# Kernel optimization log

Measured on AMD Instinct MI355X. Metric: run time of the kernel, lower is better.

The kernel has to match this reference:

```python
import jax, jax.numpy as jnp
import numpy as np

DIM = 512
HEADS = 8
SCALE = (DIM // HEADS) ** -0.5  # 0.125
B, H, W = 1, 64, 64  # square spatial grid required by torch matmul broadcasting


def setup_inputs() -> dict:
    key = jax.random.key(0)
    ks = jax.random.split(key, 7)
    s = DIM ** -0.5
    return {
        "x": jax.random.normal(ks[0], (B, H, W, DIM), dtype=jnp.float32),
        "mask": 0,  # sentinel for None (mask must be None in the original)
        "Wq": jax.random.normal(ks[1], (DIM, DIM), dtype=jnp.float32) * s,
        "bq": jax.random.normal(ks[2], (DIM,), dtype=jnp.float32) * 0.01,
        "Wk": jax.random.normal(ks[3], (DIM, DIM), dtype=jnp.float32) * s,
        "bk": jax.random.normal(ks[4], (DIM,), dtype=jnp.float32) * 0.01,
        "Wv": jax.random.normal(ks[5], (DIM, DIM), dtype=jnp.float32) * s,
        "bv": jax.random.normal(ks[6], (DIM,), dtype=jnp.float32) * 0.01,
    }


def reference(x, mask, Wq, bq, Wk, bk, Wv, bv):
    # Linear projections (nn.Linear: x @ W.T + b)
    q = jnp.einsum('bhwc,oc->bhwo', x, Wq) + bq
    k = jnp.einsum('bhwc,oc->bhwo', x, Wk) + bk
    v = jnp.einsum('bhwc,oc->bhwo', x, Wv) + bv
    # Faithful to torch.einsum('bhwc,bpqd->bhwpq', q, k): c and d are each
    # summed independently => outer product of channel-sums. [b,h,w,p,q]
    weights = jnp.einsum('bhwc,bpqd->bhwpq', q, k)
    # dropout is identity in eval mode; then scale and softmax over last axis
    weights = jax.nn.softmax(weights * SCALE, axis=-1)
    # torch matmul broadcasting: [b,h,w,p,q] @ [b,p,q,d] -> [b,h,w,p,d]
    attn = jnp.matmul(weights, v)
    return attn
```

## Files before the change

### kernel.cpp

```cpp
#include <hip/hip_runtime.h>

typedef _Float16 half8 __attribute__((ext_vector_type(8)));
typedef float f32x4 __attribute__((ext_vector_type(4)));
typedef float float4_t __attribute__((ext_vector_type(4)));
typedef unsigned int uint32x2 __attribute__((ext_vector_type(2)));

#define DIM 512
#define S 64
#define NROW 4096
#define LDSW 88

__device__ __forceinline__ void bar_lds() {
    asm volatile("s_waitcnt lgkmcnt(0)" ::: "memory");
    __builtin_amdgcn_s_barrier();
    asm volatile("" ::: "memory");
}

__global__ void colsum_vt_kernel(const float* __restrict__ Wq, const float* __restrict__ bq,
                                 const float* __restrict__ Wk, const float* __restrict__ bk,
                                 float* __restrict__ part,
                                 float* __restrict__ pbias,
                                 const float* __restrict__ X,
                                 const float* __restrict__ Wv,
                                 const float* __restrict__ bv,
                                 _Float16* __restrict__ Vs) {
    int bid = blockIdx.x;
    if (bid < 8) {
        int sel = bid >> 2, qr = bid & 3;
        const float* W = sel ? Wk : Wq;
        const float* bias = sel ? bk : bq;
        int t = threadIdx.x;
        int c0 = t, c1 = t + 256;
        float s0 = 0.f, s1 = 0.f;
        const float* Wr = W + (size_t)qr * 128 * DIM;
        for (int o = 0; o < 128; ++o) {
            s0 += Wr[o * DIM + c0];
            s1 += Wr[o * DIM + c1];
        }
        part[(sel * 4 + qr) * 512 + c0] = s0;
        part[(sel * 4 + qr) * 512 + c1] = s1;
        if (qr == 0) {
            float bs = bias[c0] + bias[c1];
#pragma unroll
            for (int off = 32; off >= 1; off >>= 1) bs += __shfl_xor(bs, off);
            __shared__ float red[4];
            if ((t & 63) == 0) red[t >> 6] = bs;
            __syncthreads();
            if (t == 0) pbias[sel] = red[0] + red[1] + red[2] + red[3];
        }
        return;
    }
    int b2 = bid - 8;
    int mb = b2 & 255;
    int cb = b2 >> 8;
    int wv_ = threadIdx.x >> 6;
    int lane = threadIdx.x & 63;
    int lr = lane & 15;
    int lg = lane >> 4;
    int row0 = mb * 16;
    int col0 = cb * 256 + wv_ * 64;

    f32x4 acc[4];
#pragma unroll
    for (int n = 0; n < 4; n++) acc[n] = (f32x4){0.f, 0.f, 0.f, 0.f};

    for (int kk = 0; kk < 16; ++kk) {
        int kbase = kk * 32 + lg * 8;
        const float4_t* pa = (const float4_t*)(X + (size_t)(row0 + lr) * DIM + kbase);
        float4_t x0 = pa[0], x1 = pa[1];
        half8 a;
#pragma unroll
        for (int i = 0; i < 4; i++) { a[i] = (_Float16)x0[i]; a[i + 4] = (_Float16)x1[i]; }
#pragma unroll
        for (int n = 0; n < 4; n++) {
            const float4_t* pb = (const float4_t*)(Wv + (size_t)(col0 + n * 16 + lr) * DIM + kbase);
            float4_t b0 = pb[0], b1 = pb[1];
            half8 hb;
#pragma unroll
            for (int i = 0; i < 4; i++) { hb[i] = (_Float16)b0[i]; hb[i + 4] = (_Float16)b1[i]; }
            acc[n] = __builtin_amdgcn_mfma_f32_16x16x32_f16(a, hb, acc[n], 0, 0, 0);
        }
    }
    int w   = mb >> 2;
    int s_  = (mb & 3) >> 1;
    int lg2 = ((mb & 3) * 2 + (lg >> 1)) & 3;
    int e0  = (lg & 1) * 4;
#pragma unroll
    for (int n = 0; n < 4; n++) {
        int d = col0 + n * 16 + lr;
        int dt = d >> 4;
        float bvc = bv[d];
        _Float16 tmp[4];
#pragma unroll
        for (int r = 0; r < 4; r++) tmp[r] = (_Float16)(acc[n][r] + bvc);
        int idx8 = (((w * 32 + dt) * 2 + s_) * 4 + lg2) * 16 + lr;
        __builtin_nontemporal_store(*(uint32x2*)tmp, (uint32x2*)(Vs + (size_t)idx8 * 8 + e0));
    }
}

__global__ void rowdot_kernel(const float* __restrict__ X,
                              const float* __restrict__ part,
                              const float* __restrict__ pbias,
                              float* __restrict__ a_arr,
                              float* __restrict__ ks_arr) {
    int wave = threadIdx.x >> 6;
    int lane = threadIdx.x & 63;
    int row = blockIdx.x * 4 + wave;
    const float4_t* xr = (const float4_t*)(X + (size_t)row * DIM) + lane * 2;
    float4_t x0 = xr[0], x1 = xr[1];
    float sq = 0.f, sk = 0.f;
#pragma unroll
    for (int qr = 0; qr < 4; ++qr) {
        const float4_t* pq = (const float4_t*)(part + qr * 512) + lane * 2;
        const float4_t* pk = (const float4_t*)(part + 2048 + qr * 512) + lane * 2;
        float4_t q0 = pq[0], q1 = pq[1];
        float4_t k0 = pk[0], k1 = pk[1];
#pragma unroll
        for (int i = 0; i < 4; i++) {
            sq += x0[i] * q0[i] + x1[i] * q1[i];
            sk += x0[i] * k0[i] + x1[i] * k1[i];
        }
    }
#pragma unroll
    for (int off = 32; off >= 1; off >>= 1) {
        sq += __shfl_xor(sq, off);
        sk += __shfl_xor(sk, off);
    }
    if (lane == 0) {
        a_arr[row]  = (sq + pbias[0]) * 0.125f;
        ks_arr[row] = sk + pbias[1];
    }
}

__global__ __launch_bounds__(256) void attn_main_kernel(
        const float* __restrict__ a_arr,
        const float* __restrict__ ks_arr,
        const _Float16* __restrict__ Vs,
        float* __restrict__ out) {
    __shared__ __align__(16) char smem[32768];
    _Float16* Wsm = (_Float16*)smem;
    char* Osm = smem;

    int b = blockIdx.x;
    int l = (b & 7) * 256 + (b >> 3);
    int w = l >> 5;
    int h0 = (l & 31) * 2;
    int t = threadIdx.x;
    int wv_ = t >> 6, lane = t & 63;
    int lr = lane & 15, lg = lane >> 4;

    const half8* Vg = (const half8*)Vs;

    half8 vfr[4][2][2];
#pragma unroll
    for (int j2 = 0; j2 < 4; ++j2)
#pragma unroll
        for (int c = 0; c < 2; ++c) {
            int dt = j2 * 8 + wv_ * 2 + c;
            int g0 = ((w * 32 + dt) * 2) * 64 + lane;
            vfr[j2][c][0] = Vg[g0];
            vfr[j2][c][1] = Vg[g0 + 64];
        }

    float a0 = a_arr[h0 * 64 + w];
    float a1 = a_arr[(h0 + 1) * 64 + w];

    for (int hh = 0; hh < 2; ++hh) {
        float a = hh ? a1 : a0;
        int hw = (h0 + hh) * 64 + w;

        bar_lds();

        {
            int p = t >> 2, c = t & 3;
            const float4_t* kp = (const float4_t*)(ks_arr + p * 64 + c * 16);
            float4_t k0 = kp[0], k1 = kp[1], k2 = kp[2], k3 = kp[3];
            float L[16];
#pragma unroll
            for (int i = 0; i < 4; i++) {
                L[i] = a * k0[i]; L[4 + i] = a * k1[i];
                L[8 + i] = a * k2[i]; L[12 + i] = a * k3[i];
            }
            float m = L[0];
#pragma unroll
            for (int i = 1; i < 16; i++) m = fmaxf(m, L[i]);
            m = fmaxf(m, __shfl_xor(m, 1));
            m = fmaxf(m, __shfl_xor(m, 2));
            float e[16];
            float sum = 0.f;
#pragma unroll
            for (int i = 0; i < 16; i++) { e[i] = __expf(L[i] - m); sum += e[i]; }
            sum += __shfl_xor(sum, 1);
            sum += __shfl_xor(sum, 2);
            float r = 1.0f / sum;
            half8 hv0, hv1;
#pragma unroll
            for (int i = 0; i < 8; i++) {
                hv0[i] = (_Float16)(e[i] * r);
                hv1[i] = (_Float16)(e[8 + i] * r);
            }
            *(half8*)&Wsm[p * LDSW + c * 16]     = hv0;
            *(half8*)&Wsm[p * LDSW + c * 16 + 8] = hv1;
        }
        bar_lds();

        half8 wfr[4][2];
#pragma unroll
        for (int pt = 0; pt < 4; ++pt)
#pragma unroll
            for (int s_ = 0; s_ < 2; ++s_)
                wfr[pt][s_] = *(const half8*)&Wsm[(pt * 16 + lr) * LDSW + s_ * 32 + lg * 8];

        char* outb = (char*)(out + (size_t)hw * (64 * DIM));

#pragma unroll
        for (int j2 = 0; j2 < 4; ++j2) {
            f32x4 acc[2][4];
#pragma unroll
            for (int c = 0; c < 2; ++c)
#pragma unroll
                for (int pt = 0; pt < 4; ++pt) acc[c][pt] = (f32x4){0.f, 0.f, 0.f, 0.f};
#pragma unroll
            for (int pt = 0; pt < 4; ++pt) {
                acc[0][pt] = __builtin_amdgcn_mfma_f32_16x16x32_f16(vfr[j2][0][0], wfr[pt][0], acc[0][pt], 0, 0, 0);
                acc[0][pt] = __builtin_amdgcn_mfma_f32_16x16x32_f16(vfr[j2][0][1], wfr[pt][1], acc[0][pt], 0, 0, 0);
                acc[1][pt] = __builtin_amdgcn_mfma_f32_16x16x32_f16(vfr[j2][1][0], wfr[pt][0], acc[1][pt], 0, 0, 0);
                acc[1][pt] = __builtin_amdgcn_mfma_f32_16x16x32_f16(vfr[j2][1][1], wfr[pt][1], acc[1][pt], 0, 0, 0);
            }
            bar_lds();
#pragma unroll
            for (int c = 0; c < 2; ++c)
#pragma unroll
                for (int pt = 0; pt < 4; ++pt) {
                    int p = pt * 16 + lr;
                    int addr = p * 512 + (wv_ * 32 + c * 16 + lg * 4) * 4;
                    addr ^= (p & 7) << 4;
                    *(f32x4*)(Osm + addr) = acc[c][pt];
                }
            bar_lds();
#pragma unroll
            for (int i = 0; i < 8; ++i) {
                int f = i * 4096 + t * 16;
                int row = f >> 9;
                int rb = f ^ ((row & 7) << 4);
                f32x4 val = *(const f32x4*)(Osm + rb);
                __builtin_nontemporal_store(val, (f32x4*)(outb + (size_t)row * 2048 + j2 * 512 + (f & 511)));
            }
        }
    }
}

extern "C" void kernel_launch(void* const* d_in, const int* in_sizes, int n_in,
                              void* d_out, int out_size, void* d_ws, size_t ws_size,
                              hipStream_t stream) {
    const float* x  = (const float*)d_in[0];
    const float* Wq = (const float*)d_in[2];
    const float* bq = (const float*)d_in[3];
    const float* Wk = (const float*)d_in[4];
    const float* bk = (const float*)d_in[5];
    const float* Wv = (const float*)d_in[6];
    const float* bv = (const float*)d_in[7];
    float* out = (float*)d_out;
    char* ws = (char*)d_ws;

    _Float16* Vs  = (_Float16*)ws;
    float* a_arr  = (float*)(ws + 4194304);
    float* ks_arr = (float*)(ws + 4210688);
    float* part   = (float*)(ws + 4227072);
    float* pbias  = (float*)(ws + 4243456);

    colsum_vt_kernel<<<520, 256, 0, stream>>>(Wq, bq, Wk, bk, part, pbias, x, Wv, bv, Vs);
    rowdot_kernel<<<1024, 256, 0, stream>>>(x, part, pbias, a_arr, ks_arr);
    attn_main_kernel<<<2048, 256, 0, stream>>>(a_arr, ks_arr, Vs, out);
}
```

Before: 139.9 us.

## Process one spatial position per block and stream V fragments per tile

The attention kernel now handles one (h,w) position per block instead of two and doubles the grid. V fragments are loaded one d-tile group at a time, just before use, instead of all being preloaded into registers. The launch bound asks for four blocks per CU. The aim is to cut register pressure and raise occupancy so more output stores are in flight, at the cost of re-reading V for every position and recomputing nothing else.

```diff
diff --git a/kernel.cpp b/kernel.cpp
--- a/kernel.cpp
+++ b/kernel.cpp
@@ -132,7 +132,7 @@
     }
 }
 
-__global__ __launch_bounds__(256) void attn_main_kernel(
+__global__ __launch_bounds__(256, 4) void attn_main_kernel(
         const float* __restrict__ a_arr,
         const float* __restrict__ ks_arr,
         const _Float16* __restrict__ Vs,
@@ -142,110 +142,105 @@
     char* Osm = smem;
 
     int b = blockIdx.x;
-    int l = (b & 7) * 256 + (b >> 3);
-    int w = l >> 5;
-    int h0 = (l & 31) * 2;
+    int swz = (b & 7) * 512 + (b >> 3);
+    int w = swz >> 6;
+    int h = swz & 63;
+    int hw = h * 64 + w;
     int t = threadIdx.x;
     int wv_ = t >> 6, lane = t & 63;
     int lr = lane & 15, lg = lane >> 4;
 
     const half8* Vg = (const half8*)Vs;
 
-    half8 vfr[4][2][2];
-#pragma unroll
-    for (int j2 = 0; j2 < 4; ++j2)
-#pragma unroll
-        for (int c = 0; c < 2; ++c) {
-            int dt = j2 * 8 + wv_ * 2 + c;
-            int g0 = ((w * 32 + dt) * 2) * 64 + lane;
-            vfr[j2][c][0] = Vg[g0];
-            vfr[j2][c][1] = Vg[g0 + 64];
-        }
-
-    float a0 = a_arr[h0 * 64 + w];
-    float a1 = a_arr[(h0 + 1) * 64 + w];
-
-    for (int hh = 0; hh < 2; ++hh) {
-        float a = hh ? a1 : a0;
-        int hw = (h0 + hh) * 64 + w;
-
+    int dtb = wv_ * 2;
+    half8 vc0 = Vg[((w * 32 + dtb) * 2 + 0) * 64 + lane];
+    half8 vc1 = Vg[((w * 32 + dtb) * 2 + 1) * 64 + lane];
+    half8 vc2 = Vg[((w * 32 + dtb + 1) * 2 + 0) * 64 + lane];
+    half8 vc3 = Vg[((w * 32 + dtb + 1) * 2 + 1) * 64 + lane];
+
+    float a = a_arr[hw];
+
+    {
+        int p = t >> 2, c = t & 3;
+        const float4_t* kp = (const float4_t*)(ks_arr + p * 64 + c * 16);
+        float4_t k0 = kp[0], k1 = kp[1], k2 = kp[2], k3 = kp[3];
+        float L[16];
+#pragma unroll
+        for (int i = 0; i < 4; i++) {
+            L[i] = a * k0[i]; L[4 + i] = a * k1[i];
+            L[8 + i] = a * k2[i]; L[12 + i] = a * k3[i];
+        }
+        float m = L[0];
+#pragma unroll
+        for (int i = 1; i < 16; i++) m = fmaxf(m, L[i]);
+        m = fmaxf(m, __shfl_xor(m, 1));
+        m = fmaxf(m, __shfl_xor(m, 2));
+        float e[16];
+        float sum = 0.f;
+#pragma unroll
+        for (int i = 0; i < 16; i++) { e[i] = __expf(L[i] - m); sum += e[i]; }
+        sum += __shfl_xor(sum, 1);
+        sum += __shfl_xor(sum, 2);
+        float r = 1.0f / sum;
+        half8 h0, h1;
+#pragma unroll
+        for (int i = 0; i < 8; i++) {
+            h0[i] = (_Float16)(e[i] * r);
+            h1[i] = (_Float16)(e[8 + i] * r);
+        }
+        *(half8*)&Wsm[p * LDSW + c * 16]     = h0;
+        *(half8*)&Wsm[p * LDSW + c * 16 + 8] = h1;
+    }
+    bar_lds();
+
+    half8 wfr[4][2];
+#pragma unroll
+    for (int pt = 0; pt < 4; ++pt)
+#pragma unroll
+        for (int s_ = 0; s_ < 2; ++s_)
+            wfr[pt][s_] = *(const half8*)&Wsm[(pt * 16 + lr) * LDSW + s_ * 32 + lg * 8];
+
+    char* outb = (char*)(out + (size_t)hw * (64 * DIM));
+
+#pragma unroll
+    for (int j2 = 0; j2 < 4; ++j2) {
+        f32x4 acc[2][4];
+#pragma unroll
+        for (int c = 0; c < 2; ++c)
+#pragma unroll
+            for (int pt = 0; pt < 4; ++pt) acc[c][pt] = (f32x4){0.f, 0.f, 0.f, 0.f};
+#pragma unroll
+        for (int pt = 0; pt < 4; ++pt) {
+            acc[0][pt] = __builtin_amdgcn_mfma_f32_16x16x32_f16(vc0, wfr[pt][0], acc[0][pt], 0, 0, 0);
+            acc[0][pt] = __builtin_amdgcn_mfma_f32_16x16x32_f16(vc1, wfr[pt][1], acc[0][pt], 0, 0, 0);
+            acc[1][pt] = __builtin_amdgcn_mfma_f32_16x16x32_f16(vc2, wfr[pt][0], acc[1][pt], 0, 0, 0);
+            acc[1][pt] = __builtin_amdgcn_mfma_f32_16x16x32_f16(vc3, wfr[pt][1], acc[1][pt], 0, 0, 0);
+        }
+        if (j2 < 3) {
+            int dt0 = (j2 + 1) * 8 + dtb;
+            vc0 = Vg[((w * 32 + dt0) * 2 + 0) * 64 + lane];
+            vc1 = Vg[((w * 32 + dt0) * 2 + 1) * 64 + lane];
+            vc2 = Vg[((w * 32 + dt0 + 1) * 2 + 0) * 64 + lane];
+            vc3 = Vg[((w * 32 + dt0 + 1) * 2 + 1) * 64 + lane];
+        }
         bar_lds();
-
-        {
-            int p = t >> 2, c = t & 3;
-            const float4_t* kp = (const float4_t*)(ks_arr + p * 64 + c * 16);
-            float4_t k0 = kp[0], k1 = kp[1], k2 = kp[2], k3 = kp[3];
-            float L[16];
-#pragma unroll
-            for (int i = 0; i < 4; i++) {
-                L[i] = a * k0[i]; L[4 + i] = a * k1[i];
-                L[8 + i] = a * k2[i]; L[12 + i] = a * k3[i];
+#pragma unroll
+        for (int c = 0; c < 2; ++c)
+#pragma unroll
+            for (int pt = 0; pt < 4; ++pt) {
+                int p = pt * 16 + lr;
+                int addr = p * 512 + (wv_ * 32 + c * 16 + lg * 4) * 4;
+                addr ^= (p & 7) << 4;
+                *(f32x4*)(Osm + addr) = acc[c][pt];
             }
-            float m = L[0];
-#pragma unroll
-            for (int i = 1; i < 16; i++) m = fmaxf(m, L[i]);
-            m = fmaxf(m, __shfl_xor(m, 1));
-            m = fmaxf(m, __shfl_xor(m, 2));
-            float e[16];
-            float sum = 0.f;
-#pragma unroll
-            for (int i = 0; i < 16; i++) { e[i] = __expf(L[i] - m); sum += e[i]; }
-            sum += __shfl_xor(sum, 1);
-            sum += __shfl_xor(sum, 2);
-            float r = 1.0f / sum;
-            half8 hv0, hv1;
-#pragma unroll
-            for (int i = 0; i < 8; i++) {
-                hv0[i] = (_Float16)(e[i] * r);
-                hv1[i] = (_Float16)(e[8 + i] * r);
-            }
-            *(half8*)&Wsm[p * LDSW + c * 16]     = hv0;
-            *(half8*)&Wsm[p * LDSW + c * 16 + 8] = hv1;
-        }
         bar_lds();
-
-        half8 wfr[4][2];
-#pragma unroll
-        for (int pt = 0; pt < 4; ++pt)
-#pragma unroll
-            for (int s_ = 0; s_ < 2; ++s_)
-                wfr[pt][s_] = *(const half8*)&Wsm[(pt * 16 + lr) * LDSW + s_ * 32 + lg * 8];
-
-        char* outb = (char*)(out + (size_t)hw * (64 * DIM));
-
-#pragma unroll
-        for (int j2 = 0; j2 < 4; ++j2) {
-            f32x4 acc[2][4];
-#pragma unroll
-            for (int c = 0; c < 2; ++c)
-#pragma unroll
-                for (int pt = 0; pt < 4; ++pt) acc[c][pt] = (f32x4){0.f, 0.f, 0.f, 0.f};
-#pragma unroll
-            for (int pt = 0; pt < 4; ++pt) {
-                acc[0][pt] = __builtin_amdgcn_mfma_f32_16x16x32_f16(vfr[j2][0][0], wfr[pt][0], acc[0][pt], 0, 0, 0);
-                acc[0][pt] = __builtin_amdgcn_mfma_f32_16x16x32_f16(vfr[j2][0][1], wfr[pt][1], acc[0][pt], 0, 0, 0);
-                acc[1][pt] = __builtin_amdgcn_mfma_f32_16x16x32_f16(vfr[j2][1][0], wfr[pt][0], acc[1][pt], 0, 0, 0);
-                acc[1][pt] = __builtin_amdgcn_mfma_f32_16x16x32_f16(vfr[j2][1][1], wfr[pt][1], acc[1][pt], 0, 0, 0);
-            }
-            bar_lds();
-#pragma unroll
-            for (int c = 0; c < 2; ++c)
-#pragma unroll
-                for (int pt = 0; pt < 4; ++pt) {
-                    int p = pt * 16 + lr;
-                    int addr = p * 512 + (wv_ * 32 + c * 16 + lg * 4) * 4;
-                    addr ^= (p & 7) << 4;
-                    *(f32x4*)(Osm + addr) = acc[c][pt];
-                }
-            bar_lds();
-#pragma unroll
-            for (int i = 0; i < 8; ++i) {
-                int f = i * 4096 + t * 16;
-                int row = f >> 9;
-                int rb = f ^ ((row & 7) << 4);
-                f32x4 val = *(const f32x4*)(Osm + rb);
-                __builtin_nontemporal_store(val, (f32x4*)(outb + (size_t)row * 2048 + j2 * 512 + (f & 511)));
-            }
+#pragma unroll
+        for (int i = 0; i < 8; ++i) {
+            int f = i * 4096 + t * 16;
+            int row = f >> 9;
+            int rb = f ^ ((row & 7) << 4);
+            f32x4 val = *(const f32x4*)(Osm + rb);
+            __builtin_nontemporal_store(val, (f32x4*)(outb + (size_t)row * 2048 + j2 * 512 + (f & 511)));
         }
     }
 }
@@ -271,5 +266,5 @@
 
     colsum_vt_kernel<<<520, 256, 0, stream>>>(Wq, bq, Wk, bk, part, pbias, x, Wv, bv, Vs);
     rowdot_kernel<<<1024, 256, 0, stream>>>(x, part, pbias, a_arr, ks_arr);
-    attn_main_kernel<<<2048, 256, 0, stream>>>(a_arr, ks_arr, Vs, out);
-}
+    attn_main_kernel<<<4096, 256, 0, stream>>>(a_arr, ks_arr, Vs, out);
+}
```

New measurement: 144.4 us. 1.03x slower.

## Give each wave a private LDS slice and drop block-wide barriers

Applied to the files above, without the earlier changes.

Repartitions the attention kernel so each wavefront owns 16 rows of p and its own 8KB LDS slice. Each wave computes the softmax weights for its rows, stages them, and transposes output tiles through its private slice, so the s_barrier calls are replaced by lgkmcnt waits plus scheduling barriers. V fragments are now loaded per j2 chunk and prefetched for the next chunk during the second h iteration, which trades register footprint for a reload per chunk. The aim is to remove block-wide synchronisation stalls between the MFMA and store phases. Correctness relies on each wave reading only the LDS data it wrote itself.

```diff
diff --git a/kernel.cpp b/kernel.cpp
--- a/kernel.cpp
+++ b/kernel.cpp
@@ -10,10 +10,10 @@
 #define NROW 4096
 #define LDSW 88
 
-__device__ __forceinline__ void bar_lds() {
+__device__ __forceinline__ void fence_lds() {
+    __builtin_amdgcn_sched_barrier(0);
     asm volatile("s_waitcnt lgkmcnt(0)" ::: "memory");
-    __builtin_amdgcn_s_barrier();
-    asm volatile("" ::: "memory");
+    __builtin_amdgcn_sched_barrier(0);
 }
 
 __global__ void colsum_vt_kernel(const float* __restrict__ Wq, const float* __restrict__ bq,
@@ -138,113 +138,110 @@
         const _Float16* __restrict__ Vs,
         float* __restrict__ out) {
     __shared__ __align__(16) char smem[32768];
-    _Float16* Wsm = (_Float16*)smem;
-    char* Osm = smem;
-
     int b = blockIdx.x;
     int l = (b & 7) * 256 + (b >> 3);
     int w = l >> 5;
     int h0 = (l & 31) * 2;
     int t = threadIdx.x;
-    int wv_ = t >> 6, lane = t & 63;
+    int wid = t >> 6, lane = t & 63;
     int lr = lane & 15, lg = lane >> 4;
 
+    char* slice = smem + wid * 8192;
+    _Float16* Wsm = (_Float16*)slice;
+    char* Osm = slice;
+
     const half8* Vg = (const half8*)Vs;
 
-    half8 vfr[4][2][2];
-#pragma unroll
-    for (int j2 = 0; j2 < 4; ++j2)
-#pragma unroll
-        for (int c = 0; c < 2; ++c) {
-            int dt = j2 * 8 + wv_ * 2 + c;
-            int g0 = ((w * 32 + dt) * 2) * 64 + lane;
-            vfr[j2][c][0] = Vg[g0];
-            vfr[j2][c][1] = Vg[g0 + 64];
-        }
-
-    float a0 = a_arr[h0 * 64 + w];
-    float a1 = a_arr[(h0 + 1) * 64 + w];
-
+    half8 vfr[8][2];
+#pragma unroll
+    for (int j = 0; j < 8; ++j) {
+        int g0 = ((w * 32 + j) * 2) * 64 + lane;
+        vfr[j][0] = Vg[g0];
+        vfr[j][1] = Vg[g0 + 64];
+    }
+
+    float av[2];
+    av[0] = a_arr[h0 * 64 + w];
+    av[1] = a_arr[(h0 + 1) * 64 + w];
+
+    half8 wfr[2][2];
+#pragma unroll
     for (int hh = 0; hh < 2; ++hh) {
-        float a = hh ? a1 : a0;
-        int hw = (h0 + hh) * 64 + w;
-
-        bar_lds();
-
-        {
-            int p = t >> 2, c = t & 3;
-            const float4_t* kp = (const float4_t*)(ks_arr + p * 64 + c * 16);
-            float4_t k0 = kp[0], k1 = kp[1], k2 = kp[2], k3 = kp[3];
-            float L[16];
-#pragma unroll
-            for (int i = 0; i < 4; i++) {
-                L[i] = a * k0[i]; L[4 + i] = a * k1[i];
-                L[8 + i] = a * k2[i]; L[12 + i] = a * k3[i];
-            }
-            float m = L[0];
-#pragma unroll
-            for (int i = 1; i < 16; i++) m = fmaxf(m, L[i]);
-            m = fmaxf(m, __shfl_xor(m, 1));
-            m = fmaxf(m, __shfl_xor(m, 2));
-            float e[16];
-            float sum = 0.f;
-#pragma unroll
-            for (int i = 0; i < 16; i++) { e[i] = __expf(L[i] - m); sum += e[i]; }
-            sum += __shfl_xor(sum, 1);
-            sum += __shfl_xor(sum, 2);
-            float r = 1.0f / sum;
-            half8 hv0, hv1;
-#pragma unroll
-            for (int i = 0; i < 8; i++) {
-                hv0[i] = (_Float16)(e[i] * r);
-                hv1[i] = (_Float16)(e[8 + i] * r);
-            }
-            *(half8*)&Wsm[p * LDSW + c * 16]     = hv0;
-            *(half8*)&Wsm[p * LDSW + c * 16 + 8] = hv1;
-        }
-        bar_lds();
-
-        half8 wfr[4][2];
-#pragma unroll
-        for (int pt = 0; pt < 4; ++pt)
-#pragma unroll
-            for (int s_ = 0; s_ < 2; ++s_)
-                wfr[pt][s_] = *(const half8*)&Wsm[(pt * 16 + lr) * LDSW + s_ * 32 + lg * 8];
-
-        char* outb = (char*)(out + (size_t)hw * (64 * DIM));
-
-#pragma unroll
-        for (int j2 = 0; j2 < 4; ++j2) {
-            f32x4 acc[2][4];
-#pragma unroll
-            for (int c = 0; c < 2; ++c)
-#pragma unroll
-                for (int pt = 0; pt < 4; ++pt) acc[c][pt] = (f32x4){0.f, 0.f, 0.f, 0.f};
-#pragma unroll
-            for (int pt = 0; pt < 4; ++pt) {
-                acc[0][pt] = __builtin_amdgcn_mfma_f32_16x16x32_f16(vfr[j2][0][0], wfr[pt][0], acc[0][pt], 0, 0, 0);
-                acc[0][pt] = __builtin_amdgcn_mfma_f32_16x16x32_f16(vfr[j2][0][1], wfr[pt][1], acc[0][pt], 0, 0, 0);
-                acc[1][pt] = __builtin_amdgcn_mfma_f32_16x16x32_f16(vfr[j2][1][0], wfr[pt][0], acc[1][pt], 0, 0, 0);
-                acc[1][pt] = __builtin_amdgcn_mfma_f32_16x16x32_f16(vfr[j2][1][1], wfr[pt][1], acc[1][pt], 0, 0, 0);
-            }
-            bar_lds();
-#pragma unroll
-            for (int c = 0; c < 2; ++c)
-#pragma unroll
-                for (int pt = 0; pt < 4; ++pt) {
-                    int p = pt * 16 + lr;
-                    int addr = p * 512 + (wv_ * 32 + c * 16 + lg * 4) * 4;
-                    addr ^= (p & 7) << 4;
-                    *(f32x4*)(Osm + addr) = acc[c][pt];
+        float a = av[hh];
+        int pl = lane >> 2, c = lane & 3;
+        const float4_t* kp = (const float4_t*)(ks_arr + (wid * 16 + pl) * 64 + c * 16);
+        float4_t k0 = kp[0], k1 = kp[1], k2 = kp[2], k3 = kp[3];
+        float L[16];
+#pragma unroll
+        for (int i = 0; i < 4; i++) {
+            L[i] = a * k0[i]; L[4 + i] = a * k1[i];
+            L[8 + i] = a * k2[i]; L[12 + i] = a * k3[i];
+        }
+        float m = L[0];
+#pragma unroll
+        for (int i = 1; i < 16; i++) m = fmaxf(m, L[i]);
+        m = fmaxf(m, __shfl_xor(m, 1));
+        m = fmaxf(m, __shfl_xor(m, 2));
+        float e[16];
+        float sum = 0.f;
+#pragma unroll
+        for (int i = 0; i < 16; i++) { e[i] = __expf(L[i] - m); sum += e[i]; }
+        sum += __shfl_xor(sum, 1);
+        sum += __shfl_xor(sum, 2);
+        float r = 1.0f / sum;
+        half8 hv0, hv1;
+#pragma unroll
+        for (int i = 0; i < 8; i++) {
+            hv0[i] = (_Float16)(e[i] * r);
+            hv1[i] = (_Float16)(e[8 + i] * r);
+        }
+        fence_lds();
+        *(half8*)&Wsm[pl * LDSW + c * 16]     = hv0;
+        *(half8*)&Wsm[pl * LDSW + c * 16 + 8] = hv1;
+        fence_lds();
+        wfr[hh][0] = *(const half8*)&Wsm[lr * LDSW + lg * 8];
+        wfr[hh][1] = *(const half8*)&Wsm[lr * LDSW + 32 + lg * 8];
+    }
+
+    char* outb[2];
+    outb[0] = (char*)(out + (size_t)(h0 * 64 + w) * (64 * DIM)) + wid * 16 * 2048;
+    outb[1] = (char*)(out + (size_t)((h0 + 1) * 64 + w) * (64 * DIM)) + wid * 16 * 2048;
+
+#pragma unroll
+    for (int j2 = 0; j2 < 4; ++j2) {
+#pragma unroll
+        for (int hh = 0; hh < 2; ++hh) {
+            f32x4 acc[8];
+#pragma unroll
+            for (int j = 0; j < 8; ++j) acc[j] = (f32x4){0.f, 0.f, 0.f, 0.f};
+#pragma unroll
+            for (int j = 0; j < 8; ++j) {
+                acc[j] = __builtin_amdgcn_mfma_f32_16x16x32_f16(vfr[j][0], wfr[hh][0], acc[j], 0, 0, 0);
+                acc[j] = __builtin_amdgcn_mfma_f32_16x16x32_f16(vfr[j][1], wfr[hh][1], acc[j], 0, 0, 0);
+            }
+            if (hh == 1 && j2 < 3) {
+#pragma unroll
+                for (int j = 0; j < 8; ++j) {
+                    int g0 = ((w * 32 + (j2 + 1) * 8 + j) * 2) * 64 + lane;
+                    vfr[j][0] = Vg[g0];
+                    vfr[j][1] = Vg[g0 + 64];
                 }
-            bar_lds();
+            }
+            fence_lds();
+#pragma unroll
+            for (int j = 0; j < 8; ++j) {
+                int addr = lr * 512 + (j * 16 + lg * 4) * 4;
+                addr ^= (lr & 7) << 4;
+                *(f32x4*)(Osm + addr) = acc[j];
+            }
+            fence_lds();
 #pragma unroll
             for (int i = 0; i < 8; ++i) {
-                int f = i * 4096 + t * 16;
+                int f = i * 1024 + lane * 16;
                 int row = f >> 9;
                 int rb = f ^ ((row & 7) << 4);
                 f32x4 val = *(const f32x4*)(Osm + rb);
-                __builtin_nontemporal_store(val, (f32x4*)(outb + (size_t)row * 2048 + j2 * 512 + (f & 511)));
+                __builtin_nontemporal_store(val, (f32x4*)(outb[hh] + (size_t)row * 2048 + j2 * 512 + (f & 511)));
             }
         }
     }
```

New measurement: 142.1 us. No clear change (+1.6%).
